# Performance work log

Measured on AMD Instinct MI355X. Metric: run time of the kernel, lower is better.

Reference implementation:

```python
import jax, jax.numpy as jnp
import numpy as np

B, S, D, H = 4, 2048, 1024, 16
DK = D // H


def setup_inputs() -> dict:
    key = jax.random.key(0)
    ks = jax.random.split(key, 7)
    xq = jax.random.normal(ks[0], (B, S, D), dtype=jnp.float32)
    xk = jax.random.normal(ks[1], (B, S, D), dtype=jnp.float32)
    xv = jax.random.normal(ks[2], (B, S, D), dtype=jnp.float32)
    attention_mask = jnp.ones((B, S), dtype=jnp.int32)  # all-valid padding mask
    scale = 0.02
    Wq = jax.random.normal(ks[3], (D, D), dtype=jnp.float32) * scale
    Wk = jax.random.normal(ks[4], (D, D), dtype=jnp.float32) * scale
    Wv = jax.random.normal(ks[5], (D, D), dtype=jnp.float32) * scale
    Wo = jax.random.normal(ks[6], (D, D), dtype=jnp.float32) * scale
    return {"x_query": xq, "x_key": xk, "x_value": xv,
            "attention_mask": attention_mask,
            "Wq": Wq, "Wk": Wk, "Wv": Wv, "Wo": Wo}


def reference(x_query, x_key, x_value, attention_mask, Wq, Wk, Wv, Wo):
    b, sq, d = x_query.shape
    sk = x_key.shape[1]
    # nn.Linear(bias=False): y = x @ W.T
    Q = x_query @ Wq.T
    K = x_key @ Wk.T
    V = x_value @ Wv.T
    # torch .split(dk, dim=-1) -> contiguous head slices == reshape (B,S,H,DK)
    Qh = Q.reshape(b, sq, H, DK).transpose(0, 2, 1, 3)  # (B,H,Sq,DK)
    Kh = K.reshape(b, sk, H, DK).transpose(0, 2, 1, 3)
    Vh = V.reshape(b, sk, H, DK).transpose(0, 2, 1, 3)
    scores = jnp.einsum('bhqd,bhkd->bhqk', Qh, Kh) / jnp.sqrt(
        jnp.asarray(DK, dtype=Qh.dtype))
    # causal mask (mask_future=True)
    causal = jnp.tril(jnp.ones((sq, sk), dtype=bool))
    scores = jnp.where(causal[None, None, :, :], scores, -jnp.inf)
    # padding mask (B,Sk) -> (B,1,1,Sk)
    pad = (attention_mask != 0)[:, None, None, :]
    scores = jnp.where(pad, scores, -jnp.inf)
    attn = jax.nn.softmax(scores, axis=-1)
    out = jnp.einsum('bhqk,bhkd->bhqd', attn, Vh)  # (B,H,Sq,DK)
    out = out.transpose(0, 2, 1, 3).reshape(b, sq, d)
    return out @ Wo.T
```

## Files before the change

### kernel.cpp

```cpp
#include <hip/hip_runtime.h>
#include <stdint.h>

#define BB 4
#define SS 2048
#define DD 1024
#define HH 16
#define DKK 64

typedef unsigned short u16;
typedef short s16x8 __attribute__((ext_vector_type(8)));
typedef float f32x4 __attribute__((ext_vector_type(4)));

__device__ __forceinline__ void async_copy16(const void* g, void* l) {
  __builtin_amdgcn_global_load_lds(
      (const __attribute__((address_space(1))) void*)g,
      (__attribute__((address_space(3))) void*)l, 16, 0, 0);
}

__device__ __forceinline__ u16 f2bf(float f) {
  union { float f; uint32_t u; } x; x.f = f;
  uint32_t r = x.u + 0x7fffu + ((x.u >> 16) & 1u);
  return (u16)(r >> 16);
}

__device__ __forceinline__ uint32_t cvtpk(float a, float b) {
  uint32_t d;
  asm("v_cvt_pk_bf16_f32 %0, %1, %2" : "=v"(d) : "v"(a), "v"(b));
  return d;
}

__device__ __forceinline__ uint32_t swz16(uint32_t x) {
  return (uint32_t)__builtin_amdgcn_ds_swizzle((int)x, 0x401F);
}

__global__ __launch_bounds__(256) void cvt_kernel(
    const float* __restrict__ x0, const float* __restrict__ x1,
    const float* __restrict__ x2, const float* __restrict__ w0,
    const float* __restrict__ w1, const float* __restrict__ w2,
    const float* __restrict__ w3, u16* __restrict__ dst) {
  const size_t base = ((size_t)blockIdx.x * 256 + threadIdx.x) * 8;
  const float* src;
  size_t off;
  if (base < 25165824ull) {
    const size_t t = base >> 23;
    src = (t == 0) ? x0 : (t == 1) ? x1 : x2;
    off = base & 8388607ull;
  } else {
    const size_t r = base - 25165824ull;
    const size_t t = r >> 20;
    src = (t == 0) ? w0 : (t == 1) ? w1 : (t == 2) ? w2 : w3;
    off = r & 1048575ull;
  }
  const float4 a = *(const float4*)(src + off);
  const float4 b = *(const float4*)(src + off + 4);
  s16x8 o;
  o[0] = (short)f2bf(a.x); o[1] = (short)f2bf(a.y);
  o[2] = (short)f2bf(a.z); o[3] = (short)f2bf(a.w);
  o[4] = (short)f2bf(b.x); o[5] = (short)f2bf(b.y);
  o[6] = (short)f2bf(b.z); o[7] = (short)f2bf(b.w);
  *(s16x8*)(dst + base) = o;
}

template <bool IN_F32, bool OUT_F32>
__global__ __launch_bounds__(256, 3) void gemm_bt(
    const void* __restrict__ Ap, const void* __restrict__ Bp, void* __restrict__ Cp,
    size_t asegstride, size_t bsegstride, size_t csegstride, int vt_seg) {
  const int K = 1024, N = 1024;
  __shared__ u16 Alds[128 * 64];
  __shared__ u16 Blds[128 * 64];
  const int tid = threadIdx.x;
  const int wid = tid >> 6, lane = tid & 63;
  const int quad = lane >> 4, l16 = lane & 15;
  const int bidx = blockIdx.x;
  const int swz = ((bidx & 7) << 6) | (bidx >> 3);
  const int mtile = swz >> 3;
  const int ntile = swz & 7;
  const int wm = wid >> 1, wn = wid & 1;
  const int seg = blockIdx.y;
  f32x4 acc[4][4] = {};
  for (int kb = 0; kb < K; kb += 64) {
    if constexpr (IN_F32) {
      const float* Af = (const float*)Ap + seg * asegstride + (size_t)mtile * 128 * K;
      const float* Bf = (const float*)Bp + seg * bsegstride + (size_t)ntile * 128 * K;
#pragma unroll
      for (int i = 0; i < 8; ++i) {
        const int c = i * 256 + tid;
        const int row = c >> 4, g = c & 15;
        const int cc = g >> 1, h = g & 1;
        const int sl = row * 8 + (cc ^ (row & 7));
        {
          const float4 v = *(const float4*)(Af + (size_t)row * K + kb + g * 4);
          ushort4 o;
          o.x = f2bf(v.x); o.y = f2bf(v.y); o.z = f2bf(v.z); o.w = f2bf(v.w);
          *(ushort4*)&Alds[sl * 8 + h * 4] = o;
        }
        {
          const float4 v = *(const float4*)(Bf + (size_t)row * K + kb + g * 4);
          ushort4 o;
          o.x = f2bf(v.x); o.y = f2bf(v.y); o.z = f2bf(v.z); o.w = f2bf(v.w);
          *(ushort4*)&Blds[sl * 8 + h * 4] = o;
        }
      }
    } else {
      const u16* Ab = (const u16*)Ap + seg * asegstride + (size_t)mtile * 128 * K;
      const u16* Bb = (const u16*)Bp + seg * bsegstride + (size_t)ntile * 128 * K;
#pragma unroll
      for (int i = 0; i < 4; ++i) {
        const int s = i * 256 + tid;
        const int row = s >> 3;
        const int cc = (s & 7) ^ (row & 7);
        async_copy16(Ab + (size_t)row * K + kb + cc * 8,
                     (char*)Alds + (i * 256 + wid * 64) * 16);
        async_copy16(Bb + (size_t)row * K + kb + cc * 8,
                     (char*)Blds + (i * 256 + wid * 64) * 16);
      }
    }
    __syncthreads();
#pragma unroll
    for (int ks = 0; ks < 2; ++ks) {
      s16x8 af[4], bfr[4];
#pragma unroll
      for (int i = 0; i < 4; ++i) {
        const int R = wm * 64 + i * 16 + l16;
        af[i] = *(const s16x8*)&Alds[(R * 8 + ((ks * 4 + quad) ^ (l16 & 7))) * 8];
      }
#pragma unroll
      for (int j = 0; j < 4; ++j) {
        const int R = wn * 64 + j * 16 + l16;
        bfr[j] = *(const s16x8*)&Blds[(R * 8 + ((ks * 4 + quad) ^ (l16 & 7))) * 8];
      }
#pragma unroll
      for (int i = 0; i < 4; ++i)
#pragma unroll
        for (int j = 0; j < 4; ++j)
          acc[i][j] = __builtin_amdgcn_mfma_f32_16x16x32_bf16(af[i], bfr[j], acc[i][j], 0, 0, 0);
    }
    __syncthreads();
  }
  const int row0 = mtile * 128 + wm * 64 + quad * 4;
  const int col0 = ntile * 128 + wn * 64 + l16;
  if (seg == vt_seg) {
    u16* VT = (u16*)Cp + (size_t)seg * csegstride;
#pragma unroll
    for (int i = 0; i < 4; ++i)
#pragma unroll
      for (int j = 0; j < 4; ++j) {
        const int col = col0 + j * 16;
        const int row = row0 + i * 16;
        const int bb = row >> 11, s0 = row & 2047;
        const size_t dst = (((size_t)bb * HH + (col >> 6)) * DKK + (col & 63)) * SS + s0;
        ushort4 o;
        o.x = f2bf(acc[i][j][0]); o.y = f2bf(acc[i][j][1]);
        o.z = f2bf(acc[i][j][2]); o.w = f2bf(acc[i][j][3]);
        *(ushort4*)(VT + dst) = o;
      }
  } else {
#pragma unroll
    for (int i = 0; i < 4; ++i)
#pragma unroll
      for (int j = 0; j < 4; ++j)
#pragma unroll
        for (int r = 0; r < 4; ++r) {
          const size_t idx = (size_t)(row0 + i * 16 + r) * N + col0 + j * 16;
          if constexpr (OUT_F32) ((float*)Cp)[seg * csegstride + idx] = acc[i][j][r];
          else                   ((u16*)Cp)[seg * csegstride + idx] = f2bf(acc[i][j][r]);
        }
  }
}

template <int MODE>
__global__ __launch_bounds__(256, 4) void attn_kernel(
    const u16* __restrict__ Q, const u16* __restrict__ K, const u16* __restrict__ VT,
    const int* __restrict__ mask, u16* __restrict__ O,
    float* __restrict__ Opart, float* __restrict__ lpart) {
  __shared__ u16 Klds[64 * 64];
  __shared__ u16 Vt[64 * 64];
  __shared__ float bias[64];
  const int bid = blockIdx.x;
  int qt, kt0, kt1, code, bh;
  if constexpr (MODE == 0) {
    qt = 15 - (bid >> 6);
    bh = bid & 63;
    code = 2;
    kt0 = 0; kt1 = 2 * qt + 2;
  } else {
    bh = bid & 63;
    const int w = bid >> 6;
    const int wsel = w >> 3, wo = w & 7;
    const uint32_t qw = (wsel == 0) ? 0xDD6EE7FFu : (wsel == 1) ? 0x4AABB5CCu : 0x01238899u;
    const uint32_t sw = (wsel == 0) ? 0x4924u : (wsel == 1) ? 0x9124u : 0xAA44u;
    qt = (int)((qw >> (wo * 4)) & 15u);
    code = (int)((sw >> (wo * 2)) & 3u);
    const int half = qt + 1;
    kt0 = (code == 1) ? half : 0;
    kt1 = (code == 0) ? half : 2 * qt + 2;
  }
  const int b = bh >> 4;
  const int h = bh & 15;
  const int tid = threadIdx.x;
  const int wid = tid >> 6, lane = tid & 63;
  const int quad = lane >> 4, l16 = lane & 15;
  const int q0 = qt * 128;
  const u16* Qb = Q + ((size_t)b * SS + q0) * DD + h * DKK;
  const u16* Kb0 = K + (size_t)b * SS * DD + h * DKK;
  const u16* VTb = VT + ((size_t)(b * HH + h)) * DKK * SS;
  s16x8 qf[2][2];
#pragma unroll
  for (int rg = 0; rg < 2; ++rg)
#pragma unroll
    for (int ks = 0; ks < 2; ++ks)
      qf[rg][ks] = *(const s16x8*)(Qb + (size_t)(wid * 32 + rg * 16 + l16) * DD +
                                   ks * 32 + quad * 8);
  s16x8 onesf;
#pragma unroll
  for (int i = 0; i < 8; ++i) onesf[i] = (short)0x3F80;
  f32x4 oacc[2][4] = {};
  f32x4 lacc[2] = {};
  const float c_scale = 0.18033688f;
  const bool qodd = (quad & 1) != 0;
  const bool is_hi = (lane >= 32);
  const bool midq = (quad == 1) || (quad == 2);
  const int xaddr = (lane ^ 32) << 2;
  const int qrow0 = q0 + wid * 32 + l16;
  auto mixf = [&](uint32_t vj0, uint32_t vj1) -> uint32_t {
    const uint32_t S  = is_hi ? vj1 : vj0;
    const uint32_t S2 = is_hi ? vj0 : vj1;
    const uint32_t R  = (uint32_t)__builtin_amdgcn_ds_bpermute(xaddr, (int)S2);
    return midq ? R : S;
  };
  for (int kt = kt0; kt < kt1; ++kt) {
    const u16* Kb = Kb0 + (size_t)(kt * 64) * DD;
#pragma unroll
    for (int i = 0; i < 2; ++i) {
      const int s = i * 256 + tid;
      const int row = s >> 3;
      const int cc = (s & 7) ^ (row & 7);
      async_copy16(Kb + (size_t)row * DD + cc * 8,
                   (char*)Klds + (i * 256 + wid * 64) * 16);
    }
#pragma unroll
    for (int i = 0; i < 2; ++i) {
      const int s = i * 256 + tid;
      const int row = s >> 3;
      const int cc = (s & 7) ^ (row & 7);
      async_copy16(VTb + (size_t)row * SS + kt * 64 + cc * 8,
                   (char*)Vt + ((i * 256 + wid * 64) * 16));
    }
    if (tid < 64) bias[tid] = mask[(size_t)b * SS + kt * 64 + tid] ? 0.0f : -1e30f;
    __syncthreads();
    f32x4 bj[4];
#pragma unroll
    for (int j = 0; j < 4; ++j) bj[j] = *(const f32x4*)&bias[j * 16 + quad * 4];
    f32x4 st[2][4] = {};
#pragma unroll
    for (int ks = 0; ks < 2; ++ks) {
      s16x8 kf[4];
#pragma unroll
      for (int j = 0; j < 4; ++j) {
        const int R = j * 16 + l16;
        kf[j] = *(const s16x8*)&Klds[(R * 8 + ((ks * 4 + quad) ^ (l16 & 7))) * 8];
      }
#pragma unroll
      for (int rg = 0; rg < 2; ++rg)
#pragma unroll
        for (int j = 0; j < 4; ++j)
          st[rg][j] = __builtin_amdgcn_mfma_f32_16x16x32_bf16(kf[j], qf[rg][ks],
                                                              st[rg][j], 0, 0, 0);
    }
    const bool causal = (kt >= 2 * qt);
    uint32_t pkv[2][8];
#pragma unroll
    for (int rg = 0; rg < 2; ++rg) {
      const int qrow = qrow0 + rg * 16;
#pragma unroll
      for (int j = 0; j < 4; ++j) {
        float p[4];
#pragma unroll
        for (int r = 0; r < 4; ++r) {
          float v = __builtin_amdgcn_exp2f(st[rg][j][r] * c_scale + bj[j][r]);
          if (causal && (kt * 64 + j * 16 + quad * 4 + r) > qrow) v = 0.0f;
          p[r] = v;
        }
        pkv[rg][j * 2 + 0] = cvtpk(p[0], p[1]);
        pkv[rg][j * 2 + 1] = cvtpk(p[2], p[3]);
      }
    }
#pragma unroll
    for (int ks = 0; ks < 2; ++ks) {
      const int j0 = ks * 2, j1 = ks * 2 + 1;
      s16x8 pf[2];
#pragma unroll
      for (int rg = 0; rg < 2; ++rg) {
        const uint32_t Xa0 = pkv[rg][j0 * 2 + 0], Xa1 = pkv[rg][j0 * 2 + 1];
        const uint32_t Xb0 = pkv[rg][j1 * 2 + 0], Xb1 = pkv[rg][j1 * 2 + 1];
        const uint32_t Pa0 = swz16(Xa0), Pa1 = swz16(Xa1);
        const uint32_t Pb0 = swz16(Xb0), Pb1 = swz16(Xb1);
        const uint32_t Ea0 = qodd ? Pa0 : Xa0, Oa0 = qodd ? Xa0 : Pa0;
        const uint32_t Ea1 = qodd ? Pa1 : Xa1, Oa1 = qodd ? Xa1 : Pa1;
        const uint32_t Eb0 = qodd ? Pb0 : Xb0, Ob0 = qodd ? Xb0 : Pb0;
        const uint32_t Eb1 = qodd ? Pb1 : Xb1, Ob1 = qodd ? Xb1 : Pb1;
        union { uint32_t w[4]; s16x8 v; } u;
        u.w[0] = mixf(Ea0, Eb0);
        u.w[1] = mixf(Ea1, Eb1);
        u.w[2] = mixf(Oa0, Ob0);
        u.w[3] = mixf(Oa1, Ob1);
        pf[rg] = u.v;
      }
#pragma unroll
      for (int jt = 0; jt < 4; ++jt) {
        const int d = jt * 16 + l16;
        const s16x8 vf = *(const s16x8*)&Vt[(d * 8 + ((ks * 4 + quad) ^ (d & 7))) * 8];
#pragma unroll
        for (int rg = 0; rg < 2; ++rg)
          oacc[rg][jt] = __builtin_amdgcn_mfma_f32_16x16x32_bf16(pf[rg], vf,
                                                                oacc[rg][jt], 0, 0, 0);
      }
#pragma unroll
      for (int rg = 0; rg < 2; ++rg)
        lacc[rg] = __builtin_amdgcn_mfma_f32_16x16x32_bf16(pf[rg], onesf, lacc[rg],
                                                           0, 0, 0);
    }
    __syncthreads();
  }
  if (code == 2) {
    u16* Ob = O + ((size_t)b * SS + q0) * DD + h * DKK;
#pragma unroll
    for (int rg = 0; rg < 2; ++rg)
#pragma unroll
      for (int r = 0; r < 4; ++r) {
        const float inv = 1.0f / lacc[rg][r];
        const int row = wid * 32 + rg * 16 + quad * 4 + r;
#pragma unroll
        for (int jt = 0; jt < 4; ++jt)
          Ob[(size_t)row * DD + jt * 16 + l16] = f2bf(oacc[rg][jt][r] * inv);
      }
  } else {
    const int tile = (bh << 3) + (qt - 8);
    const int p = tile * 2 + code;
    float* Op = Opart + (size_t)p * 8192;
    float* lp = lpart + (size_t)p * 128;
#pragma unroll
    for (int rg = 0; rg < 2; ++rg)
#pragma unroll
      for (int r = 0; r < 4; ++r) {
        const int row = wid * 32 + rg * 16 + quad * 4 + r;
        if (l16 == 0) lp[row] = lacc[rg][r];
#pragma unroll
        for (int jt = 0; jt < 4; ++jt)
          Op[row * 64 + jt * 16 + l16] = oacc[rg][jt][r];
      }
  }
}

__global__ __launch_bounds__(256) void combine_kernel(
    const float* __restrict__ Opart, const float* __restrict__ lpart,
    u16* __restrict__ O) {
  const int tile = blockIdx.x;
  const int bh = tile >> 3;
  const int qt = (tile & 7) + 8;
  const int b = bh >> 4, h = bh & 15;
  const int tid = threadIdx.x;
  const int row = tid >> 1;
  const int c0 = (tid & 1) * 32;
  const float* P0 = Opart + ((size_t)tile * 2 + 0) * 8192 + row * 64 + c0;
  const float* P1 = Opart + ((size_t)tile * 2 + 1) * 8192 + row * 64 + c0;
  const float l = lpart[((size_t)tile * 2 + 0) * 128 + row] +
                  lpart[((size_t)tile * 2 + 1) * 128 + row];
  const float inv = 1.0f / l;
  u16* Ob = O + ((size_t)b * SS + qt * 128 + row) * DD + h * DKK + c0;
#pragma unroll
  for (int i = 0; i < 8; ++i) {
    const f32x4 a = *(const f32x4*)(P0 + i * 4);
    const f32x4 c = *(const f32x4*)(P1 + i * 4);
    ushort4 o;
    o.x = f2bf((a[0] + c[0]) * inv); o.y = f2bf((a[1] + c[1]) * inv);
    o.z = f2bf((a[2] + c[2]) * inv); o.w = f2bf((a[3] + c[3]) * inv);
    *(ushort4*)(Ob + i * 4) = o;
  }
}

extern "C" void kernel_launch(void* const* d_in, const int* in_sizes, int n_in,
                              void* d_out, int out_size, void* d_ws, size_t ws_size,
                              hipStream_t stream) {
  const float* xq = (const float*)d_in[0];
  const float* xk = (const float*)d_in[1];
  const float* xv = (const float*)d_in[2];
  const int* mask = (const int*)d_in[3];
  const float* Wq = (const float*)d_in[4];
  const float* Wk = (const float*)d_in[5];
  const float* Wv = (const float*)d_in[6];
  const float* Wo = (const float*)d_in[7];
  float* out = (float*)d_out;
  const size_t elems = (size_t)BB * SS * DD;
  const size_t welems = (size_t)DD * DD;
  if (ws_size >= 109051904ull) {
    u16* wsb = (u16*)d_ws;
    u16* Xq = wsb;
    u16* Wqb = wsb + 3 * elems;
    u16* Wob = Wqb + 3 * welems;
    u16* Qb = wsb + 3 * elems + 4 * welems;
    u16* Kb = Qb + elems;
    u16* Vb = Kb + elems;
    u16* Ob = wsb;
    float* Opart = (float*)(wsb + elems);
    float* lpart = (float*)(wsb + 3 * elems);
    cvt_kernel<<<14336, 256, 0, stream>>>(xq, xk, xv, Wq, Wk, Wv, Wo, wsb);
    gemm_bt<false, false><<<dim3(512, 3), 256, 0, stream>>>(
        Xq, Wqb, Qb, elems, welems, elems, 2);
    attn_kernel<1><<<1536, 256, 0, stream>>>(Qb, Kb, Vb, mask, Ob, Opart, lpart);
    combine_kernel<<<512, 256, 0, stream>>>(Opart, lpart, Ob);
    gemm_bt<false, true><<<dim3(512, 1), 256, 0, stream>>>(Ob, Wob, out, 0, 0, 0, -1);
  } else {
    u16* Qb = (u16*)d_ws;
    u16* Kb = Qb + elems;
    u16* Vb = Kb + elems;
    u16* Ob = Vb + elems;
    gemm_bt<true, false><<<dim3(512, 1), 256, 0, stream>>>(xq, Wq, Qb, 0, 0, 0, -1);
    gemm_bt<true, false><<<dim3(512, 1), 256, 0, stream>>>(xk, Wk, Kb, 0, 0, 0, -1);
    gemm_bt<true, false><<<dim3(512, 1), 256, 0, stream>>>(xv, Wv, Vb, 0, 0, 0, 0);
    attn_kernel<0><<<1024, 256, 0, stream>>>(Qb, Kb, Vb, mask, Ob,
                                             (float*)d_ws, (float*)d_ws);
    gemm_bt<false, true><<<dim3(512, 1), 256, 0, stream>>>(Ob, Wo, out, 0, 0, 0, -1);
  }
}
```

Baseline: 314.8 us.

## Double-buffer K/V tiles in attention kernel and load mask directly to registers

Splits the K and V LDS tiles into two buffers and issues the async loads for the next key tile before computing on the current one, waiting with a partial vmcnt count instead of a full __syncthreads. The padding-mask bias is now read from global memory straight into registers rather than staged through shared memory. The goal is to hide global-load latency behind the MFMA work. In exchange it doubles the LDS footprint, which may cut occupancy, and relies on hand-counted vmcnt values that must match the exact number of outstanding loads.

```diff
diff --git a/kernel.cpp b/kernel.cpp
--- a/kernel.cpp
+++ b/kernel.cpp
@@ -173,9 +173,8 @@
     const u16* __restrict__ Q, const u16* __restrict__ K, const u16* __restrict__ VT,
     const int* __restrict__ mask, u16* __restrict__ O,
     float* __restrict__ Opart, float* __restrict__ lpart) {
-  __shared__ u16 Klds[64 * 64];
-  __shared__ u16 Vt[64 * 64];
-  __shared__ float bias[64];
+  __shared__ u16 Klds[2][64 * 64];
+  __shared__ u16 Vt[2][64 * 64];
   const int bid = blockIdx.x;
   int qt, kt0, kt1, code, bh;
   if constexpr (MODE == 0) {
@@ -204,6 +203,7 @@
   const u16* Qb = Q + ((size_t)b * SS + q0) * DD + h * DKK;
   const u16* Kb0 = K + (size_t)b * SS * DD + h * DKK;
   const u16* VTb = VT + ((size_t)(b * HH + h)) * DKK * SS;
+  const int* mrow = mask + (size_t)b * SS;
   s16x8 qf[2][2];
 #pragma unroll
   for (int rg = 0; rg < 2; ++rg)
@@ -228,7 +228,7 @@
     const uint32_t R  = (uint32_t)__builtin_amdgcn_ds_bpermute(xaddr, (int)S2);
     return midq ? R : S;
   };
-  for (int kt = kt0; kt < kt1; ++kt) {
+  auto stage = [&](int bufsel, int kt) {
     const u16* Kb = Kb0 + (size_t)(kt * 64) * DD;
 #pragma unroll
     for (int i = 0; i < 2; ++i) {
@@ -236,7 +236,7 @@
       const int row = s >> 3;
       const int cc = (s & 7) ^ (row & 7);
       async_copy16(Kb + (size_t)row * DD + cc * 8,
-                   (char*)Klds + (i * 256 + wid * 64) * 16);
+                   (char*)(&Klds[bufsel][0]) + (i * 256 + wid * 64) * 16);
     }
 #pragma unroll
     for (int i = 0; i < 2; ++i) {
@@ -244,13 +244,30 @@
       const int row = s >> 3;
       const int cc = (s & 7) ^ (row & 7);
       async_copy16(VTb + (size_t)row * SS + kt * 64 + cc * 8,
-                   (char*)Vt + ((i * 256 + wid * 64) * 16));
-    }
-    if (tid < 64) bias[tid] = mask[(size_t)b * SS + kt * 64 + tid] ? 0.0f : -1e30f;
-    __syncthreads();
+                   (char*)(&Vt[bufsel][0]) + (i * 256 + wid * 64) * 16);
+    }
+  };
+
+  stage(kt0 & 1, kt0);
+  for (int kt = kt0; kt < kt1; ++kt) {
+    const int cur = kt & 1;
+    int4 mq[4];
+#pragma unroll
+    for (int j = 0; j < 4; ++j)
+      mq[j] = *(const int4*)(mrow + kt * 64 + j * 16 + quad * 4);
+    __builtin_amdgcn_sched_barrier(0);
+    const int ktn = (kt + 1 < kt1) ? kt + 1 : kt;
+    stage(cur ^ 1, ktn);
+    __builtin_amdgcn_sched_barrier(0);
+    asm volatile("s_waitcnt vmcnt(4)\n\ts_barrier" ::: "memory");
     f32x4 bj[4];
 #pragma unroll
-    for (int j = 0; j < 4; ++j) bj[j] = *(const f32x4*)&bias[j * 16 + quad * 4];
+    for (int j = 0; j < 4; ++j) {
+      bj[j][0] = mq[j].x ? 0.0f : -1e30f;
+      bj[j][1] = mq[j].y ? 0.0f : -1e30f;
+      bj[j][2] = mq[j].z ? 0.0f : -1e30f;
+      bj[j][3] = mq[j].w ? 0.0f : -1e30f;
+    }
     f32x4 st[2][4] = {};
 #pragma unroll
     for (int ks = 0; ks < 2; ++ks) {
@@ -258,7 +275,7 @@
 #pragma unroll
       for (int j = 0; j < 4; ++j) {
         const int R = j * 16 + l16;
-        kf[j] = *(const s16x8*)&Klds[(R * 8 + ((ks * 4 + quad) ^ (l16 & 7))) * 8];
+        kf[j] = *(const s16x8*)&Klds[cur][(R * 8 + ((ks * 4 + quad) ^ (l16 & 7))) * 8];
       }
 #pragma unroll
       for (int rg = 0; rg < 2; ++rg)
@@ -309,7 +326,7 @@
 #pragma unroll
       for (int jt = 0; jt < 4; ++jt) {
         const int d = jt * 16 + l16;
-        const s16x8 vf = *(const s16x8*)&Vt[(d * 8 + ((ks * 4 + quad) ^ (d & 7))) * 8];
+        const s16x8 vf = *(const s16x8*)&Vt[cur][(d * 8 + ((ks * 4 + quad) ^ (d & 7))) * 8];
 #pragma unroll
         for (int rg = 0; rg < 2; ++rg)
           oacc[rg][jt] = __builtin_amdgcn_mfma_f32_16x16x32_bf16(pf[rg], vf,
@@ -320,8 +337,9 @@
         lacc[rg] = __builtin_amdgcn_mfma_f32_16x16x32_bf16(pf[rg], onesf, lacc[rg],
                                                            0, 0, 0);
     }
-    __syncthreads();
-  }
+    asm volatile("s_barrier" ::: "memory");
+  }
+  asm volatile("s_waitcnt vmcnt(0)" ::: "memory");
   if (code == 2) {
     u16* Ob = O + ((size_t)b * SS + q0) * DD + h * DKK;
 #pragma unroll
```

New measurement: 331.9 us. 5.4% more time.
